# Kernel tuning notes

Hardware: AMD Instinct MI355X
Metric: run time of the kernel (lower is better)

## Reference

```python
import jax, jax.numpy as jnp
import numpy as np

KERNEL_SIZE = 15
PAD = (KERNEL_SIZE - 1) // 2


def _dark_channel(x):
    # x: [B, 3, H, W] in [-1, 1]
    x = (x + 1.0) / 2.0
    x = jnp.min(x, axis=1, keepdims=True)            # channel min -> [B,1,H,W]
    x = jnp.pad(x, ((0, 0), (0, 0), (PAD, PAD), (PAD, PAD)), mode='reflect')
    # sliding-window min (morphological erosion), VALID after reflect pad
    x = jax.lax.reduce_window(
        x, jnp.inf, jax.lax.min,
        window_dimensions=(1, 1, KERNEL_SIZE, KERNEL_SIZE),
        window_strides=(1, 1, 1, 1),
        padding='VALID')
    return jnp.clip(x, 0.0, 0.1)


def setup_inputs() -> dict:
    key = jax.random.key(0)
    k1, k2 = jax.random.split(key)
    shape = (16, 3, 512, 512)
    # tanh-range images in [-1, 1]
    real = jax.random.uniform(k1, shape, dtype=jnp.float32) * 2.0 - 1.0
    fake = jax.random.uniform(k2, shape, dtype=jnp.float32) * 2.0 - 1.0
    return {"real": real, "fake": fake}


def reference(real, fake):
    real_map = _dark_channel(real)
    fake_map = _dark_channel(fake)
    diff = real_map - fake_map
    return jnp.mean(diff * diff)  # nn.MSELoss (mean reduction)
```

## Files before the change

### kernel.cpp

```cpp
#include <hip/hip_runtime.h>

#define BDIM 256
#define TILE 64
#define HALO 7
#define IN_T 78
#define LSTR 79
#define IMG_H 512
#define IMG_W 512
#define NPIX (16.0f * 512.0f * 512.0f)

__device__ __forceinline__ int reflect_idx(int i, int n) {
    i = (i < 0) ? -i : i;
    i = (i >= n) ? (2 * n - 2 - i) : i;
    return i;
}

__device__ __forceinline__ void dark_tile(const float* __restrict__ X,
                                          float* __restrict__ cmin,
                                          float* __restrict__ vm,
                                          int tid, int r0g, int c0g,
                                          float (&o)[16]) {
    for (int p = tid; p < IN_T * IN_T; p += BDIM) {
        int r = (unsigned)p / IN_T;
        int c = p - r * IN_T;
        int gr = reflect_idx(r0g + r, IMG_H);
        int gc = reflect_idx(c0g + c, IMG_W);
        const float* px = X + (size_t)gr * IMG_W + gc;
        float v = fminf(px[0], fminf(px[IMG_H * IMG_W], px[2 * IMG_H * IMG_W]));
        cmin[r * LSTR + c] = v;
    }
    __syncthreads();

    for (int t = tid; t < IN_T * 4; t += BDIM) {
        int col = (unsigned)t % IN_T;
        int rr0 = ((unsigned)t / IN_T) * 16;
        float s[15];
        #pragma unroll
        for (int j = 0; j < 15; ++j) s[j] = cmin[(rr0 + j) * LSTR + col];
        #pragma unroll
        for (int j = 13; j >= 0; --j) s[j] = fminf(s[j], s[j + 1]);
        vm[rr0 * LSTR + col] = s[0];
        float f = cmin[(rr0 + 15) * LSTR + col];
        #pragma unroll
        for (int i = 1; i <= 14; ++i) {
            vm[(rr0 + i) * LSTR + col] = fminf(s[i], f);
            f = fminf(f, cmin[(rr0 + 15 + i) * LSTR + col]);
        }
        vm[(rr0 + 15) * LSTR + col] = f;
    }
    __syncthreads();

    {
        int row = tid >> 2;
        int c0 = (tid & 3) * 16;
        const float* vr = vm + row * LSTR + c0;
        float s[15];
        #pragma unroll
        for (int j = 0; j < 15; ++j) s[j] = vr[j];
        #pragma unroll
        for (int j = 13; j >= 0; --j) s[j] = fminf(s[j], s[j + 1]);
        o[0] = s[0];
        float f = vr[15];
        #pragma unroll
        for (int i = 1; i <= 14; ++i) {
            o[i] = fminf(s[i], f);
            f = fminf(f, vr[15 + i]);
        }
        o[15] = f;
    }
}

__global__ __launch_bounds__(BDIM)
void dcl_kernel(const float* __restrict__ real, const float* __restrict__ fake,
                float* __restrict__ out) {
    __shared__ float cmin[IN_T * LSTR];
    __shared__ float vm[TILE * LSTR];
    __shared__ float red[BDIM / 64];

    const int tid = threadIdx.x;
    const int r0g = blockIdx.y * TILE - HALO;
    const int c0g = blockIdx.x * TILE - HALO;
    const size_t ib = (size_t)blockIdx.z * 3 * IMG_H * IMG_W;

    float o_r[16], o_f[16];
    dark_tile(real + ib, cmin, vm, tid, r0g, c0g, o_r);
    dark_tile(fake + ib, cmin, vm, tid, r0g, c0g, o_f);

    float acc = 0.f;
    #pragma unroll
    for (int i = 0; i < 16; ++i) {
        float a = fminf(fmaxf(0.5f * o_r[i] + 0.5f, 0.f), 0.1f);
        float b = fminf(fmaxf(0.5f * o_f[i] + 0.5f, 0.f), 0.1f);
        float d = a - b;
        acc += d * d;
    }
    #pragma unroll
    for (int off = 32; off >= 1; off >>= 1)
        acc += __shfl_xor(acc, off, 64);
    if ((tid & 63) == 0) red[tid >> 6] = acc;
    __syncthreads();
    if (tid == 0) {
        float t = red[0] + red[1] + red[2] + red[3];
        atomicAdd(out, t * (1.0f / NPIX));
    }
}

extern "C" void kernel_launch(void* const* d_in, const int* in_sizes, int n_in,
                              void* d_out, int out_size, void* d_ws, size_t ws_size,
                              hipStream_t stream) {
    const float* real = (const float*)d_in[0];
    const float* fake = (const float*)d_in[1];
    float* out = (float*)d_out;
    hipMemsetAsync(out, 0, sizeof(float), stream);
    dim3 grid(IMG_W / TILE, IMG_H / TILE, 16);
    dcl_kernel<<<grid, BDIM, 0, stream>>>(real, fake, out);
}
```

Before: 145.0 us.

## Fuse channel-min and horizontal erosion into vectorized per-thread global row loads

The channel min and the horizontal 15-tap min are now computed straight from global memory. Each thread loads a 30-wide row segment with float4 vector loads, falling back to reflect-indexed scalar loads only at image borders. This removes the separate channel-min shared buffer, one shared-memory pass and one barrier per image, and shrinks LDS so more blocks can be resident. A barrier is added between the real and fake tiles because they now share one buffer. Neighbouring threads read overlapping global columns, so more bytes pass through the cache.

```diff
diff --git a/kernel.cpp b/kernel.cpp
--- a/kernel.cpp
+++ b/kernel.cpp
@@ -4,10 +4,13 @@
 #define TILE 64
 #define HALO 7
 #define IN_T 78
-#define LSTR 79
+#define LSTR 67
 #define IMG_H 512
 #define IMG_W 512
+#define HW (IMG_H * IMG_W)
 #define NPIX (16.0f * 512.0f * 512.0f)
+
+typedef float f4 __attribute__((ext_vector_type(4)));
 
 __device__ __forceinline__ int reflect_idx(int i, int n) {
     i = (i < 0) ? -i : i;
@@ -15,76 +18,95 @@
     return i;
 }
 
+__device__ __forceinline__ void hmin_row(const float* __restrict__ X, int gr,
+                                         int C0, bool fast,
+                                         float* __restrict__ dst) {
+    float w[30];
+    const float* rowp = X + (size_t)gr * IMG_W;
+    if (fast) {
+        const float* g0 = rowp + (C0 - 1);
+        #pragma unroll
+        for (int b = 0; b < 8; ++b) {
+            f4 a = *(const f4*)(g0 + 4 * b);
+            f4 g = *(const f4*)(g0 + HW + 4 * b);
+            f4 c = *(const f4*)(g0 + 2 * HW + 4 * b);
+            #pragma unroll
+            for (int k = 0; k < 4; ++k) {
+                int idx = 4 * b + k - 1;
+                if (idx >= 0 && idx < 30)
+                    w[idx] = fminf(a[k], fminf(g[k], c[k]));
+            }
+        }
+    } else {
+        #pragma unroll
+        for (int j = 0; j < 30; ++j) {
+            int gc = reflect_idx(C0 + j, IMG_W);
+            w[j] = fminf(rowp[gc], fminf(rowp[HW + gc], rowp[2 * HW + gc]));
+        }
+    }
+    float s[15];
+    #pragma unroll
+    for (int j = 0; j < 15; ++j) s[j] = w[j];
+    #pragma unroll
+    for (int j = 13; j >= 0; --j) s[j] = fminf(s[j], s[j + 1]);
+    dst[0] = s[0];
+    float f = w[15];
+    #pragma unroll
+    for (int i = 1; i <= 14; ++i) {
+        dst[i] = fminf(s[i], f);
+        f = fminf(f, w[15 + i]);
+    }
+    dst[15] = f;
+}
+
+__device__ __forceinline__ void vmin_col(const float* __restrict__ hm, int col,
+                                         int rr0, float (&o)[16]) {
+    float s[15];
+    #pragma unroll
+    for (int j = 0; j < 15; ++j) s[j] = hm[(rr0 + j) * LSTR + col];
+    #pragma unroll
+    for (int j = 13; j >= 0; --j) s[j] = fminf(s[j], s[j + 1]);
+    o[0] = s[0];
+    float f = hm[(rr0 + 15) * LSTR + col];
+    #pragma unroll
+    for (int i = 1; i <= 14; ++i) {
+        o[i] = fminf(s[i], f);
+        f = fminf(f, hm[(rr0 + 15 + i) * LSTR + col]);
+    }
+    o[15] = f;
+}
+
 __device__ __forceinline__ void dark_tile(const float* __restrict__ X,
-                                          float* __restrict__ cmin,
-                                          float* __restrict__ vm,
-                                          int tid, int r0g, int c0g,
+                                          float* __restrict__ hm,
+                                          int tid, int r0g, int c0blk,
                                           float (&o)[16]) {
-    for (int p = tid; p < IN_T * IN_T; p += BDIM) {
-        int r = (unsigned)p / IN_T;
-        int c = p - r * IN_T;
-        int gr = reflect_idx(r0g + r, IMG_H);
-        int gc = reflect_idx(c0g + c, IMG_W);
-        const float* px = X + (size_t)gr * IMG_W + gc;
-        float v = fminf(px[0], fminf(px[IMG_H * IMG_W], px[2 * IMG_H * IMG_W]));
-        cmin[r * LSTR + c] = v;
+    for (int t = tid; t < IN_T * 4; t += BDIM) {
+        int chunk = (unsigned)t / IN_T;
+        int row = t - chunk * IN_T;
+        int C0 = c0blk + chunk * 16;
+        int gr = reflect_idx(r0g + row, IMG_H);
+        bool fast = (C0 >= 1) && (C0 + 30 < IMG_W);
+        hmin_row(X, gr, C0, fast, hm + row * LSTR + chunk * 16);
     }
     __syncthreads();
-
-    for (int t = tid; t < IN_T * 4; t += BDIM) {
-        int col = (unsigned)t % IN_T;
-        int rr0 = ((unsigned)t / IN_T) * 16;
-        float s[15];
-        #pragma unroll
-        for (int j = 0; j < 15; ++j) s[j] = cmin[(rr0 + j) * LSTR + col];
-        #pragma unroll
-        for (int j = 13; j >= 0; --j) s[j] = fminf(s[j], s[j + 1]);
-        vm[rr0 * LSTR + col] = s[0];
-        float f = cmin[(rr0 + 15) * LSTR + col];
-        #pragma unroll
-        for (int i = 1; i <= 14; ++i) {
-            vm[(rr0 + i) * LSTR + col] = fminf(s[i], f);
-            f = fminf(f, cmin[(rr0 + 15 + i) * LSTR + col]);
-        }
-        vm[(rr0 + 15) * LSTR + col] = f;
-    }
-    __syncthreads();
-
-    {
-        int row = tid >> 2;
-        int c0 = (tid & 3) * 16;
-        const float* vr = vm + row * LSTR + c0;
-        float s[15];
-        #pragma unroll
-        for (int j = 0; j < 15; ++j) s[j] = vr[j];
-        #pragma unroll
-        for (int j = 13; j >= 0; --j) s[j] = fminf(s[j], s[j + 1]);
-        o[0] = s[0];
-        float f = vr[15];
-        #pragma unroll
-        for (int i = 1; i <= 14; ++i) {
-            o[i] = fminf(s[i], f);
-            f = fminf(f, vr[15 + i]);
-        }
-        o[15] = f;
-    }
+    vmin_col(hm, tid & 63, (tid >> 6) * 16, o);
 }
 
-__global__ __launch_bounds__(BDIM)
+__global__ __launch_bounds__(BDIM, 4)
 void dcl_kernel(const float* __restrict__ real, const float* __restrict__ fake,
                 float* __restrict__ out) {
-    __shared__ float cmin[IN_T * LSTR];
-    __shared__ float vm[TILE * LSTR];
+    __shared__ float hm[IN_T * LSTR];
     __shared__ float red[BDIM / 64];
 
     const int tid = threadIdx.x;
     const int r0g = blockIdx.y * TILE - HALO;
-    const int c0g = blockIdx.x * TILE - HALO;
-    const size_t ib = (size_t)blockIdx.z * 3 * IMG_H * IMG_W;
+    const int c0blk = blockIdx.x * TILE - HALO;
+    const size_t ib = (size_t)blockIdx.z * 3 * HW;
 
     float o_r[16], o_f[16];
-    dark_tile(real + ib, cmin, vm, tid, r0g, c0g, o_r);
-    dark_tile(fake + ib, cmin, vm, tid, r0g, c0g, o_f);
+    dark_tile(real + ib, hm, tid, r0g, c0blk, o_r);
+    __syncthreads();
+    dark_tile(fake + ib, hm, tid, r0g, c0blk, o_f);
 
     float acc = 0.f;
     #pragma unroll
```

After: 173.7 us. 19.8% more time.

## Store clipped dark-channel values as bf16 in LDS with vectorized loads

Applied to the files above, without the earlier changes.

The affine map and clip now happen before the erosion, which is valid because both are monotone. The clipped values are rounded to bf16 and stored as 16-bit integers, so the separable min passes use integer compares on half-size shared memory. Interior tiles load four columns at a time with float4 reads; edge tiles keep a scalar reflect path. Rounding to bf16 loses precision in the per-pixel values, which could push the MSE past tolerance, and a launch-bounds occupancy hint is also added.

```diff
diff --git a/kernel.cpp b/kernel.cpp
--- a/kernel.cpp
+++ b/kernel.cpp
@@ -4,10 +4,15 @@
 #define TILE 64
 #define HALO 7
 #define IN_T 78
-#define LSTR 79
-#define IMG_H 512
-#define IMG_W 512
+#define CSTR 84
+#define VSTR 82
+#define IMG 512
+#define HW (IMG * IMG)
 #define NPIX (16.0f * 512.0f * 512.0f)
+#define P1_TASKS (IN_T * 20)
+#define P1_ITERS 7
+
+typedef float f4 __attribute__((ext_vector_type(4)));
 
 __device__ __forceinline__ int reflect_idx(int i, int n) {
     i = (i < 0) ? -i : i;
@@ -15,83 +20,129 @@
     return i;
 }
 
+__device__ __forceinline__ unsigned short umin16(unsigned short a, unsigned short b) {
+    return a < b ? a : b;
+}
+
+__device__ __forceinline__ unsigned short map_bf16(float v) {
+    float m = fminf(fmaxf(fmaf(v, 0.5f, 0.5f), 0.0f), 0.1f);
+    unsigned int u = __float_as_uint(m);
+    return (unsigned short)((u + 0x7fffu + ((u >> 16) & 1u)) >> 16);
+}
+
+__device__ __forceinline__ float bf16_f32(unsigned short x) {
+    return __uint_as_float(((unsigned int)x) << 16);
+}
+
 __device__ __forceinline__ void dark_tile(const float* __restrict__ X,
-                                          float* __restrict__ cmin,
-                                          float* __restrict__ vm,
-                                          int tid, int r0g, int c0g,
+                                          unsigned short* __restrict__ cmin,
+                                          unsigned short* __restrict__ vm,
+                                          int tid, int r0g, int c0g, bool fastcol,
                                           float (&o)[16]) {
-    for (int p = tid; p < IN_T * IN_T; p += BDIM) {
-        int r = (unsigned)p / IN_T;
-        int c = p - r * IN_T;
-        int gr = reflect_idx(r0g + r, IMG_H);
-        int gc = reflect_idx(c0g + c, IMG_W);
-        const float* px = X + (size_t)gr * IMG_W + gc;
-        float v = fminf(px[0], fminf(px[IMG_H * IMG_W], px[2 * IMG_H * IMG_W]));
-        cmin[r * LSTR + c] = v;
+    #pragma unroll
+    for (int i = 0; i < P1_ITERS; ++i) {
+        int t = tid + i * BDIM;
+        t = t < (P1_TASKS - 1) ? t : (P1_TASKS - 1);
+        int row = (unsigned)t / 20u;
+        int g = t - row * 20;
+        int gr = reflect_idx(r0g + row, IMG);
+        const float* rp = X + (size_t)gr * IMG;
+        unsigned short w[4];
+        if (fastcol) {
+            const float* p = rp + (c0g - 1 + 4 * g);
+            f4 a = *(const f4*)p;
+            f4 b = *(const f4*)(p + HW);
+            f4 c = *(const f4*)(p + 2 * HW);
+            #pragma unroll
+            for (int k = 0; k < 4; ++k)
+                w[k] = map_bf16(fminf(a[k], fminf(b[k], c[k])));
+        } else {
+            #pragma unroll
+            for (int k = 0; k < 4; ++k) {
+                int gc = reflect_idx(c0g - 1 + 4 * g + k, IMG);
+                float v = fminf(rp[gc], fminf(rp[HW + gc], rp[2 * HW + gc]));
+                w[k] = map_bf16(v);
+            }
+        }
+        uint2 pk;
+        pk.x = (unsigned)w[0] | ((unsigned)w[1] << 16);
+        pk.y = (unsigned)w[2] | ((unsigned)w[3] << 16);
+        *(uint2*)&cmin[row * CSTR + 4 * g] = pk;
     }
     __syncthreads();
 
-    for (int t = tid; t < IN_T * 4; t += BDIM) {
-        int col = (unsigned)t % IN_T;
-        int rr0 = ((unsigned)t / IN_T) * 16;
-        float s[15];
-        #pragma unroll
-        for (int j = 0; j < 15; ++j) s[j] = cmin[(rr0 + j) * LSTR + col];
-        #pragma unroll
-        for (int j = 13; j >= 0; --j) s[j] = fminf(s[j], s[j + 1]);
-        vm[rr0 * LSTR + col] = s[0];
-        float f = cmin[(rr0 + 15) * LSTR + col];
-        #pragma unroll
-        for (int i = 1; i <= 14; ++i) {
-            vm[(rr0 + i) * LSTR + col] = fminf(s[i], f);
-            f = fminf(f, cmin[(rr0 + 15 + i) * LSTR + col]);
+    #pragma unroll
+    for (int b = 0; b < 2; ++b) {
+        int t = tid + b * BDIM;
+        if (t < IN_T * 4) {
+            int col = (unsigned)t % (unsigned)IN_T;
+            int rr0 = ((unsigned)t / (unsigned)IN_T) * 16;
+            const unsigned short* cp = cmin + (col + 1);
+            unsigned short s[15];
+            #pragma unroll
+            for (int j = 0; j < 15; ++j) s[j] = cp[(rr0 + j) * CSTR];
+            #pragma unroll
+            for (int j = 13; j >= 0; --j) s[j] = umin16(s[j], s[j + 1]);
+            unsigned short* vp = vm + col;
+            vp[rr0 * VSTR] = s[0];
+            unsigned short f = cp[(rr0 + 15) * CSTR];
+            #pragma unroll
+            for (int i2 = 1; i2 <= 14; ++i2) {
+                vp[(rr0 + i2) * VSTR] = umin16(s[i2], f);
+                f = umin16(f, cp[(rr0 + 15 + i2) * CSTR]);
+            }
+            vp[(rr0 + 15) * VSTR] = f;
         }
-        vm[(rr0 + 15) * LSTR + col] = f;
     }
     __syncthreads();
 
     {
-        int row = tid >> 2;
-        int c0 = (tid & 3) * 16;
-        const float* vr = vm + row * LSTR + c0;
-        float s[15];
+        int row = tid >> 2, k = tid & 3;
+        const unsigned int* vr = (const unsigned int*)(vm + row * VSTR) + 8 * k;
+        unsigned short x[32];
         #pragma unroll
-        for (int j = 0; j < 15; ++j) s[j] = vr[j];
+        for (int j = 0; j < 16; ++j) {
+            unsigned int d = vr[j];
+            x[2 * j] = (unsigned short)d;
+            x[2 * j + 1] = (unsigned short)(d >> 16);
+        }
+        unsigned short s[15];
         #pragma unroll
-        for (int j = 13; j >= 0; --j) s[j] = fminf(s[j], s[j + 1]);
-        o[0] = s[0];
-        float f = vr[15];
+        for (int j = 0; j < 15; ++j) s[j] = x[j];
         #pragma unroll
-        for (int i = 1; i <= 14; ++i) {
-            o[i] = fminf(s[i], f);
-            f = fminf(f, vr[15 + i]);
+        for (int j = 13; j >= 0; --j) s[j] = umin16(s[j], s[j + 1]);
+        o[0] = bf16_f32(s[0]);
+        unsigned short f = x[15];
+        #pragma unroll
+        for (int i2 = 1; i2 <= 14; ++i2) {
+            o[i2] = bf16_f32(umin16(s[i2], f));
+            f = umin16(f, x[15 + i2]);
         }
-        o[15] = f;
+        o[15] = bf16_f32(f);
     }
 }
 
-__global__ __launch_bounds__(BDIM)
+__global__ __launch_bounds__(BDIM, 4)
 void dcl_kernel(const float* __restrict__ real, const float* __restrict__ fake,
                 float* __restrict__ out) {
-    __shared__ float cmin[IN_T * LSTR];
-    __shared__ float vm[TILE * LSTR];
+    __shared__ __align__(8) unsigned short cmin[IN_T * CSTR];
+    __shared__ __align__(8) unsigned short vm[TILE * VSTR];
     __shared__ float red[BDIM / 64];
 
     const int tid = threadIdx.x;
     const int r0g = blockIdx.y * TILE - HALO;
     const int c0g = blockIdx.x * TILE - HALO;
-    const size_t ib = (size_t)blockIdx.z * 3 * IMG_H * IMG_W;
+    const bool fastcol = (c0g >= 1) && (c0g + 79 <= IMG);
+    const size_t ib = (size_t)blockIdx.z * 3 * HW;
 
     float o_r[16], o_f[16];
-    dark_tile(real + ib, cmin, vm, tid, r0g, c0g, o_r);
-    dark_tile(fake + ib, cmin, vm, tid, r0g, c0g, o_f);
+    dark_tile(real + ib, cmin, vm, tid, r0g, c0g, fastcol, o_r);
+    dark_tile(fake + ib, cmin, vm, tid, r0g, c0g, fastcol, o_f);
 
     float acc = 0.f;
     #pragma unroll
     for (int i = 0; i < 16; ++i) {
-        float a = fminf(fmaxf(0.5f * o_r[i] + 0.5f, 0.f), 0.1f);
-        float b = fminf(fmaxf(0.5f * o_f[i] + 0.5f, 0.f), 0.1f);
-        float d = a - b;
+        float d = o_r[i] - o_f[i];
         acc += d * d;
     }
     #pragma unroll
@@ -112,6 +163,6 @@
     const float* fake = (const float*)d_in[1];
     float* out = (float*)d_out;
     hipMemsetAsync(out, 0, sizeof(float), stream);
-    dim3 grid(IMG_W / TILE, IMG_H / TILE, 16);
+    dim3 grid(IMG / TILE, IMG / TILE, 16);
     dcl_kernel<<<grid, BDIM, 0, stream>>>(real, fake, out);
 }
```

New measurement: 143.5 us. Within noise of the previous version (-1.1%).
